# Kernel tuning notes

Measured on AMD Instinct MI355X. Metric: run time of the kernel, lower is better.

The kernel has to match this reference:

```python
import jax, jax.numpy as jnp
import numpy as np


def _unfold(x, ks, pad):
    # torch nn.Unfold ordering: flattened channel dim is (c, kh, kw), output (b, c*ks*ks, h*w)
    b, c, h, w = x.shape
    if ks == 1:
        return x.reshape(b, c, h * w)
    xp = jnp.pad(x, ((0, 0), (0, 0), (pad, pad), (pad, pad)))
    patches = jnp.stack([xp[:, :, i:i + h, j:j + w] for i in range(ks) for j in range(ks)], axis=2)  # (b,c,ks*ks,h,w)
    return patches.reshape(b, c * ks * ks, h * w)


def _cg_conv(x, weight, ce_w, gd_w, gd2_w, ci_w, ks, pad, g=8):
    # Content-gated conv: SE-style dynamic kernel generation + unfold + batched matmul
    b, c, h, w = x.shape
    oc = weight.shape[0]
    # AdaptiveMaxPool2d((ks,ks)); h,w divisible by ks so bins are uniform
    gl = x.reshape(b, c, ks, h // ks, ks, w // ks).max(axis=(3, 5)).reshape(b, c, ks * ks)
    ce2 = jnp.einsum('bck,nk->bcn', gl, ce_w)                      # (b,c,num_lat)
    out = jnp.einsum('bcn,kn->bck', jax.nn.relu(ce2), gd_w)        # (b,c,ks*ks)
    # channel path: (b,c//g,g,num_lat) -> transpose -> Linear(g -> oc/(c//g))
    t = jax.nn.relu(jnp.transpose(ce2.reshape(b, c // g, g, -1), (0, 1, 3, 2)))
    ocp = jnp.transpose(jnp.einsum('bpng,og->bpno', t, ci_w), (0, 1, 3, 2)).reshape(b, oc, -1)
    ocp = jnp.einsum('bon,kn->bok', jax.nn.relu(ocp), gd2_w)       # (b,oc,ks*ks)
    dyn = jax.nn.sigmoid(out[:, None, :, :] + ocp[:, :, None, :])  # (b,oc,c,ks*ks)
    dyn = dyn * weight.reshape(1, oc, c, ks * ks)
    x_un = _unfold(x, ks, pad)                                     # (b, c*ks*ks, h*w)
    y = jnp.einsum('bok,bkl->bol', dyn.reshape(b, oc, c * ks * ks), x_un)
    return y.reshape(b, oc, h, w)


def setup_inputs() -> dict:
    key = jax.random.key(0)
    ks_ = jax.random.split(key, 12)
    b, c_in, c_hid, c_out, H, W = 4, 64, 256, 64, 96, 96
    s = 0.02
    inp = {
        'x': jax.random.normal(ks_[0], (b, c_in, H, W), jnp.float32),
        # fc1: 1x1, num_lat = 1, ci: 8 -> 256//(64//8)=32
        'fc1_weight': jax.random.normal(ks_[1], (c_hid, c_in, 1, 1), jnp.float32) * s,
        'fc1_ce': jax.random.normal(ks_[2], (1, 1), jnp.float32) * s,
        'fc1_gd': jax.random.normal(ks_[3], (1, 1), jnp.float32) * s,
        'fc1_gd2': jax.random.normal(ks_[4], (1, 1), jnp.float32) * s,
        'fc1_ci': jax.random.normal(ks_[5], (32, 8), jnp.float32) * s,
        # fc2: 3x3, num_lat = 5, ci: 8 -> 64//(256//8)=2
        'fc2_weight': jax.random.normal(ks_[6], (c_out, c_hid, 3, 3), jnp.float32) * s,
        'fc2_ce': jax.random.normal(ks_[7], (5, 9), jnp.float32) * s,
        'fc2_gd': jax.random.normal(ks_[8], (9, 5), jnp.float32) * s,
        'fc2_gd2': jax.random.normal(ks_[9], (9, 5), jnp.float32) * s,
        'fc2_ci': jax.random.normal(ks_[10], (2, 8), jnp.float32) * s,
    }
    return inp


def reference(x, fc1_weight, fc1_ce, fc1_gd, fc1_gd2, fc1_ci,
              fc2_weight, fc2_ce, fc2_gd, fc2_gd2, fc2_ci):
    h = _cg_conv(x, fc1_weight, fc1_ce, fc1_gd, fc1_gd2, fc1_ci, ks=1, pad=0)
    h = jax.nn.gelu(h, approximate=False)  # torch nn.GELU default is exact erf
    return _cg_conv(h, fc2_weight, fc2_ce, fc2_gd, fc2_gd2, fc2_ci, ks=3, pad=1)
```

## Files before the change

kernel.cpp:

```cpp
#include <hip/hip_runtime.h>
#include <math.h>

typedef __attribute__((ext_vector_type(8))) short short8x;
typedef __attribute__((ext_vector_type(4))) float float4x;
typedef unsigned short u16;
typedef unsigned int u32;

__device__ __forceinline__ float bf2f(u16 u) {
    return __uint_as_float(((u32)u) << 16);
}
__device__ __forceinline__ u16 f2bf(float f) {
    u32 u = __float_as_uint(f);
    u32 r = (u + 0x7fffu + ((u >> 16) & 1u)) >> 16;
    return (u16)r;
}
__device__ __forceinline__ u32 fenc(float f) {
    u32 b = __float_as_uint(f);
    return b ^ (0x80000000u | (u32)((int)b >> 31));
}
__device__ __forceinline__ float fdec(u32 u) {
    u32 b = (u & 0x80000000u) ? (u ^ 0x80000000u) : ~u;
    return __uint_as_float(b);
}


__global__ __launch_bounds__(256) void k_gl1(const float* __restrict__ x, float* __restrict__ gl1,
                                             u32* __restrict__ h2p32, u32* __restrict__ gl2u) {
    if (blockIdx.x >= 256) {
        int t = threadIdx.x;
        int plane_id = blockIdx.x - 256;
        u32* plane = h2p32 + plane_id * (98 * 98 * 16);
        for (int i = t; i < 1568; i += 256) plane[i] = 0u;
        for (int i = t; i < 1568; i += 256) plane[97 * 98 * 16 + i] = 0u;
        for (int i = t; i < 3072; i += 256) {
            int r = (i >> 5) + 1;
            int p = ((i >> 4) & 1) * 97;
            int w = i & 15;
            plane[(r * 98 + p) * 16 + w] = 0u;
        }
        for (int i = plane_id * 288 + t; i < (plane_id + 1) * 288; i += 256)
            gl2u[i] = 0u;
        return;
    }
    int b = blockIdx.x >> 6, c = blockIdx.x & 63;
    const float4* p = (const float4*)(x + (b * 64 + c) * 9216);
    float m = -1e30f;
    #pragma unroll
    for (int i = 0; i < 9; i++) {
        float4 v = p[i * 256 + threadIdx.x];
        m = fmaxf(m, fmaxf(fmaxf(v.x, v.y), fmaxf(v.z, v.w)));
    }
    __shared__ float red[256];
    red[threadIdx.x] = m;
    __syncthreads();
    for (int s = 128; s > 0; s >>= 1) {
        if (threadIdx.x < s) red[threadIdx.x] = fmaxf(red[threadIdx.x], red[threadIdx.x + s]);
        __syncthreads();
    }
    if (threadIdx.x == 0) gl1[b * 64 + c] = red[0];
}

__global__ __launch_bounds__(256) void k_gate1(const float* __restrict__ gl1,
                                               const float* __restrict__ ce, const float* __restrict__ gd,
                                               const float* __restrict__ gd2, const float* __restrict__ ci,
                                               const float* __restrict__ w1, u16* __restrict__ W1A) {
    int b = blockIdx.x >> 4, s = blockIdx.x & 15;
    int t = threadIdx.x;
    __shared__ float rce[64], out1[64], ocp[256];
    float cew = ce[0], gdw = gd[0], gd2w = gd2[0];
    if (t < 64) {
        float r = fmaxf(gl1[b * 64 + t] * cew, 0.f);
        rce[t] = r;
        out1[t] = r * gdw;
    }
    __syncthreads();
    {
        int p = t >> 5, oi = t & 31;
        float sv = 0.f;
        #pragma unroll
        for (int g = 0; g < 8; g++) sv += rce[p * 8 + g] * ci[oi * 8 + g];
        ocp[t] = fmaxf(sv, 0.f) * gd2w;
    }
    __syncthreads();
    u16* Wb = W1A + b * 256 * 64;
    #pragma unroll
    for (int i = 0; i < 4; i++) {
        int idx = s * 1024 + i * 256 + t;
        int o = idx >> 6, c = idx & 63;
        float v = out1[c] + ocp[o];
        float sg = 1.f / (1.f + expf(-v));
        Wb[idx] = f2bf(sg * w1[idx]);
    }
}

__global__ __launch_bounds__(256) void k_gemm1(const u16* __restrict__ W1A, const float* __restrict__ x,
                                               u16* __restrict__ h2p, u32* __restrict__ gl2u) {
    int bi = blockIdx.x;
    int b = bi / 192, rem = bi % 192;
    int y = rem >> 1, half = rem & 1;
    int t = threadIdx.x, wave = t >> 6, lane = t & 63, l15 = lane & 15, quad = lane >> 4;

    __shared__ __align__(16) u16 xs[48 * 72];
    const float* xb = x + (b * 64) * 9216 + y * 96 + half * 48;
    #pragma unroll
    for (int i = 0; i < 12; i++) {
        int idx = i * 256 + t;
        int c = idx / 48, px = idx - c * 48;
        xs[px * 72 + c] = f2bf(xb[c * 9216 + px]);
    }
    __syncthreads();

    float4x acc[4][3];
    #pragma unroll
    for (int mt = 0; mt < 4; mt++)
        #pragma unroll
        for (int nt = 0; nt < 3; nt++) acc[mt][nt] = (float4x){0.f, 0.f, 0.f, 0.f};
    const u16* Wb = W1A + b * 256 * 64;
    #pragma unroll
    for (int c0 = 0; c0 < 64; c0 += 32) {
        short8x bfr[3];
        #pragma unroll
        for (int nt = 0; nt < 3; nt++)
            bfr[nt] = *(const short8x*)(xs + (nt * 16 + l15) * 72 + c0 + quad * 8);
        #pragma unroll
        for (int mt = 0; mt < 4; mt++) {
            int oc = wave * 64 + mt * 16 + l15;
            short8x afr = *(const short8x*)(Wb + oc * 64 + c0 + quad * 8);
            #pragma unroll
            for (int nt = 0; nt < 3; nt++)
                acc[mt][nt] = __builtin_amdgcn_mfma_f32_16x16x32_bf16(afr, bfr[nt], acc[mt][nt], 0, 0, 0);
        }
    }
    const float is2 = 0.70710678118654752f;
    float gf[4][3][4];
    #pragma unroll
    for (int mt = 0; mt < 4; mt++) {
        #pragma unroll
        for (int nt = 0; nt < 3; nt++) {
            int xx = half * 48 + nt * 16 + l15;
            int oc0 = wave * 64 + mt * 16 + quad * 4;
            int g = oc0 >> 5, cl = oc0 & 31;
            u16 pk[4];
            #pragma unroll
            for (int r = 0; r < 4; r++) {
                float v = acc[mt][nt][r];
                float gl = 0.5f * v * (1.f + erff(v * is2));
                gf[mt][nt][r] = gl;
                pk[r] = f2bf(gl);
            }
            u16* dst = h2p + ((((b * 8 + g) * 98 + y + 1) * 98) + xx + 1) * 32 + cl;
            *(ushort4*)dst = make_ushort4(pk[0], pk[1], pk[2], pk[3]);
        }
    }
    int ki = y >> 5;
    int kA = ki * 3 + (half == 0 ? 0 : 1);
    int kB = ki * 3 + (half == 0 ? 1 : 2);
    #pragma unroll
    for (int mt = 0; mt < 4; mt++) {
        float vA[4], vB[4];
        #pragma unroll
        for (int r = 0; r < 4; r++) {
            if (half == 0) { vA[r] = fmaxf(gf[mt][0][r], gf[mt][1][r]); vB[r] = gf[mt][2][r]; }
            else           { vA[r] = gf[mt][0][r]; vB[r] = fmaxf(gf[mt][1][r], gf[mt][2][r]); }
        }
        #pragma unroll
        for (int m = 1; m < 16; m <<= 1) {
            #pragma unroll
            for (int r = 0; r < 4; r++) {
                vA[r] = fmaxf(vA[r], __shfl_xor(vA[r], m));
                vB[r] = fmaxf(vB[r], __shfl_xor(vB[r], m));
            }
        }
        if (l15 == 0) {
            #pragma unroll
            for (int r = 0; r < 4; r++) {
                int oc = wave * 64 + mt * 16 + quad * 4 + r;
                atomicMax(&gl2u[(b * 9 + kA) * 256 + oc], fenc(vA[r]));
                atomicMax(&gl2u[(b * 9 + kB) * 256 + oc], fenc(vB[r]));
            }
        }
    }
}

__global__ __launch_bounds__(256) void k_gate2(const u32* __restrict__ gl2u,
                                               const float* __restrict__ ce, const float* __restrict__ gd,
                                               const float* __restrict__ gd2, const float* __restrict__ ci,
                                               const float* __restrict__ w2, u16* __restrict__ W2A) {
    int b = blockIdx.x >> 4, s = blockIdx.x & 15;
    int t = threadIdx.x;
    __shared__ float rce[256][5];
    __shared__ float out2[256][9];
    __shared__ float ocp2[64][9];
    {
        float gl[9];
        #pragma unroll
        for (int k = 0; k < 9; k++) gl[k] = fdec(gl2u[(b * 9 + k) * 256 + t]);
        float r[5];
        #pragma unroll
        for (int n = 0; n < 5; n++) {
            float sv = 0.f;
            #pragma unroll
            for (int k = 0; k < 9; k++) sv += gl[k] * ce[n * 9 + k];
            r[n] = fmaxf(sv, 0.f);
            rce[t][n] = r[n];
        }
        #pragma unroll
        for (int k = 0; k < 9; k++) {
            float sv = 0.f;
            #pragma unroll
            for (int n = 0; n < 5; n++) sv += r[n] * gd[k * 5 + n];
            out2[t][k] = sv;
        }
    }
    __syncthreads();
    if (t < 64) {
        int p = t >> 1, oi = t & 1;
        float rt[5];
        #pragma unroll
        for (int n = 0; n < 5; n++) {
            float sv = 0.f;
            #pragma unroll
            for (int g = 0; g < 8; g++) sv += rce[p * 8 + g][n] * ci[oi * 8 + g];
            rt[n] = fmaxf(sv, 0.f);
        }
        #pragma unroll
        for (int k = 0; k < 9; k++) {
            float sv = 0.f;
            #pragma unroll
            for (int n = 0; n < 5; n++) sv += rt[n] * gd2[k * 5 + n];
            ocp2[t][k] = sv;
        }
    }
    __syncthreads();
    u16* Wb = W2A + b * (8 * 9 * 64 * 32);
    for (int it = 0; it < 36; it++) {
        int flat = s * 9216 + it * 256 + t;
        int cl = flat & 31;
        int o = (flat >> 5) & 63;
        int rest = flat >> 11;
        int k = rest % 9, g = rest / 9;
        int c = g * 32 + cl;
        float v = out2[c][k] + ocp2[o][k];
        float sg = 1.f / (1.f + expf(-v));
        Wb[flat] = f2bf(sg * w2[(o * 256 + c) * 9 + k]);
    }
}

__global__ __launch_bounds__(128) void k_conv2(const u16* __restrict__ W2A, const u16* __restrict__ h2p,
                                               float* __restrict__ out) {
    int b = blockIdx.x / 96, y = blockIdx.x % 96;
    int t = threadIdx.x, ni = t >> 6, lane = t & 63, l15 = lane & 15, quad = lane >> 4;
    __shared__ __align__(16) u16 Als[9 * 64 * 32];
    __shared__ __align__(16) u16 Bls[3 * 98 * 32];
    float4x acc[4][3];
    #pragma unroll
    for (int mt = 0; mt < 4; mt++)
        #pragma unroll
        for (int nt = 0; nt < 3; nt++) acc[mt][nt] = (float4x){0.f, 0.f, 0.f, 0.f};

    for (int g = 0; g < 8; g++) {
        __syncthreads();
        const uint4* As = (const uint4*)(W2A + (b * 8 + g) * (9 * 64 * 32));
        uint4* Ad = (uint4*)Als;
        #pragma unroll
        for (int i = 0; i < 18; i++) Ad[t + i * 128] = As[t + i * 128];
        #pragma unroll
        for (int r = 0; r < 3; r++) {
            const uint4* Bs = (const uint4*)(h2p + (((b * 8 + g) * 98 + y + r) * 98) * 32);
            uint4* Bd = (uint4*)(Bls + r * 98 * 32);
            for (int i = t; i < 392; i += 128) Bd[i] = Bs[i];
        }
        __syncthreads();
        #pragma unroll
        for (int k = 0; k < 9; k++) {
            int ki = k / 3, kj = k - ki * 3;
            short8x af[4];
            #pragma unroll
            for (int mt = 0; mt < 4; mt++)
                af[mt] = *(const short8x*)(Als + (k * 64 + mt * 16 + l15) * 32 + quad * 8);
            #pragma unroll
            for (int nt = 0; nt < 3; nt++) {
                int px = ni * 48 + nt * 16 + l15 + kj;
                short8x bf = *(const short8x*)(Bls + (ki * 98 + px) * 32 + quad * 8);
                #pragma unroll
                for (int mt = 0; mt < 4; mt++)
                    acc[mt][nt] = __builtin_amdgcn_mfma_f32_16x16x32_bf16(af[mt], bf, acc[mt][nt], 0, 0, 0);
            }
        }
    }
    #pragma unroll
    for (int mt = 0; mt < 4; mt++) {
        #pragma unroll
        for (int nt = 0; nt < 3; nt++) {
            int xx = ni * 48 + nt * 16 + l15;
            #pragma unroll
            for (int r = 0; r < 4; r++) {
                int oc = mt * 16 + quad * 4 + r;
                out[((b * 64 + oc) * 96 + y) * 96 + xx] = acc[mt][nt][r];
            }
        }
    }
}

extern "C" void kernel_launch(void* const* d_in, const int* in_sizes, int n_in,
                              void* d_out, int out_size, void* d_ws, size_t ws_size,
                              hipStream_t stream) {
    const float* x    = (const float*)d_in[0];
    const float* w1   = (const float*)d_in[1];
    const float* ce1  = (const float*)d_in[2];
    const float* gd1  = (const float*)d_in[3];
    const float* gd21 = (const float*)d_in[4];
    const float* ci1  = (const float*)d_in[5];
    const float* w2   = (const float*)d_in[6];
    const float* ce2  = (const float*)d_in[7];
    const float* gd2  = (const float*)d_in[8];
    const float* gd22 = (const float*)d_in[9];
    const float* ci2  = (const float*)d_in[10];
    float* out = (float*)d_out;

    char* ws = (char*)d_ws;
    u16*   h2p  = (u16*)(ws + 4718592);
    u16*   W1A  = (u16*)(ws + 24387584);
    u16*   W2A  = (u16*)(ws + 24518656);
    float* gl1  = (float*)(ws + 25698304);
    u32*   gl2u = (u32*)(ws + 25796608);

    k_gl1  <<<288, 256, 0, stream>>>(x, gl1, (u32*)h2p, gl2u);
    k_gate1<<<64,  256, 0, stream>>>(gl1, ce1, gd1, gd21, ci1, w1, W1A);
    k_gemm1<<<768, 256, 0, stream>>>(W1A, x, h2p, gl2u);
    k_gate2<<<64,  256, 0, stream>>>(gl2u, ce2, gd2, gd22, ci2, w2, W2A);
    k_conv2<<<384, 128, 0, stream>>>(W2A, h2p, out);
}
```

Before: 154.8 us.

## Split conv2 rows into halves with per-wave output-channel tiles, read weights from global

New measurement: 137.8 us. 10.9% less time.

```diff
diff --git a/kernel.cpp b/kernel.cpp
--- a/kernel.cpp
+++ b/kernel.cpp
@@ -246,58 +246,46 @@
     }
 }
 
-__global__ __launch_bounds__(128) void k_conv2(const u16* __restrict__ W2A, const u16* __restrict__ h2p,
+__global__ __launch_bounds__(256) void k_conv2(const u16* __restrict__ W2A, const u16* __restrict__ h2p,
                                                float* __restrict__ out) {
-    int b = blockIdx.x / 96, y = blockIdx.x % 96;
-    int t = threadIdx.x, ni = t >> 6, lane = t & 63, l15 = lane & 15, quad = lane >> 4;
-    __shared__ __align__(16) u16 Als[9 * 64 * 32];
-    __shared__ __align__(16) u16 Bls[3 * 98 * 32];
-    float4x acc[4][3];
-    #pragma unroll
-    for (int mt = 0; mt < 4; mt++)
-        #pragma unroll
-        for (int nt = 0; nt < 3; nt++) acc[mt][nt] = (float4x){0.f, 0.f, 0.f, 0.f};
+    int bi = blockIdx.x;
+    int b = bi / 192, rem = bi % 192;
+    int y = rem >> 1, half = rem & 1;
+    int t = threadIdx.x, wave = t >> 6, lane = t & 63, l15 = lane & 15, quad = lane >> 4;
+    __shared__ __align__(16) u16 Bls[3 * 50 * 32];
+    float4x acc[3];
+    #pragma unroll
+    for (int nt = 0; nt < 3; nt++) acc[nt] = (float4x){0.f, 0.f, 0.f, 0.f};
 
     for (int g = 0; g < 8; g++) {
         __syncthreads();
-        const uint4* As = (const uint4*)(W2A + (b * 8 + g) * (9 * 64 * 32));
-        uint4* Ad = (uint4*)Als;
-        #pragma unroll
-        for (int i = 0; i < 18; i++) Ad[t + i * 128] = As[t + i * 128];
-        #pragma unroll
-        for (int r = 0; r < 3; r++) {
-            const uint4* Bs = (const uint4*)(h2p + (((b * 8 + g) * 98 + y + r) * 98) * 32);
-            uint4* Bd = (uint4*)(Bls + r * 98 * 32);
-            for (int i = t; i < 392; i += 128) Bd[i] = Bs[i];
+        const u16* plane = h2p + (b * 8 + g) * (98 * 98 * 32);
+        for (int i = t; i < 600; i += 256) {
+            int r = i / 200, c16 = i - r * 200;
+            const uint4* src = (const uint4*)(plane + ((y + r) * 98 + half * 48) * 32 + c16 * 8);
+            ((uint4*)Bls)[r * 200 + c16] = *src;
         }
         __syncthreads();
+        const u16* Wg = W2A + (b * 8 + g) * (9 * 64 * 32);
         #pragma unroll
         for (int k = 0; k < 9; k++) {
             int ki = k / 3, kj = k - ki * 3;
-            short8x af[4];
-            #pragma unroll
-            for (int mt = 0; mt < 4; mt++)
-                af[mt] = *(const short8x*)(Als + (k * 64 + mt * 16 + l15) * 32 + quad * 8);
+            short8x af = *(const short8x*)(Wg + (k * 64 + wave * 16 + l15) * 32 + quad * 8);
             #pragma unroll
             for (int nt = 0; nt < 3; nt++) {
-                int px = ni * 48 + nt * 16 + l15 + kj;
-                short8x bf = *(const short8x*)(Bls + (ki * 98 + px) * 32 + quad * 8);
-                #pragma unroll
-                for (int mt = 0; mt < 4; mt++)
-                    acc[mt][nt] = __builtin_amdgcn_mfma_f32_16x16x32_bf16(af[mt], bf, acc[mt][nt], 0, 0, 0);
+                int pxl = nt * 16 + l15 + kj;
+                short8x bf = *(const short8x*)(Bls + (ki * 50 + pxl) * 32 + quad * 8);
+                acc[nt] = __builtin_amdgcn_mfma_f32_16x16x32_bf16(af, bf, acc[nt], 0, 0, 0);
             }
         }
     }
     #pragma unroll
-    for (int mt = 0; mt < 4; mt++) {
-        #pragma unroll
-        for (int nt = 0; nt < 3; nt++) {
-            int xx = ni * 48 + nt * 16 + l15;
-            #pragma unroll
-            for (int r = 0; r < 4; r++) {
-                int oc = mt * 16 + quad * 4 + r;
-                out[((b * 64 + oc) * 96 + y) * 96 + xx] = acc[mt][nt][r];
-            }
+    for (int nt = 0; nt < 3; nt++) {
+        int xx = half * 48 + nt * 16 + l15;
+        #pragma unroll
+        for (int r = 0; r < 4; r++) {
+            int oc = wave * 16 + quad * 4 + r;
+            out[((b * 64 + oc) * 96 + y) * 96 + xx] = acc[nt][r];
         }
     }
 }
@@ -329,5 +317,5 @@
     k_gate1<<<64,  256, 0, stream>>>(gl1, ce1, gd1, gd21, ci1, w1, W1A);
     k_gemm1<<<768, 256, 0, stream>>>(W1A, x, h2p, gl2u);
     k_gate2<<<64,  256, 0, stream>>>(gl2u, ce2, gd2, gd22, ci2, w2, W2A);
-    k_conv2<<<384, 128, 0, stream>>>(W2A, h2p, out);
-}
+    k_conv2<<<768, 256, 0, stream>>>(W2A, h2p, out);
+}
```
